# Kernel tuning notes

Hardware: AMD Instinct MI355X
Metric: run time of the kernel (lower is better)

Reference implementation:

```python
import jax, jax.numpy as jnp
import numpy as np

H, RANK, BATCH, T = 1024, 4, 128, 256


def setup_inputs() -> dict:
    key = jax.random.key(0)
    ks = jax.random.split(key, 6)
    s = 1.0 / np.sqrt(H)  # glorot-ish scale for params
    return {
        "x": jax.random.normal(ks[0], (BATCH, T, H), jnp.float32),
        "h0": jnp.zeros((BATCH, H), jnp.float32),
        "d": jax.random.normal(ks[1], (H,), jnp.float32) * s,
        "L": jax.random.normal(ks[2], (H, RANK), jnp.float32) * s,
        "R": jax.random.normal(ks[3], (RANK, H), jnp.float32) * s,
        "B": jax.random.normal(ks[4], (H, H), jnp.float32) * s,
    }


def reference(x, h0, d, L, R, B):
    # Input projection B.T @ x_t for all steps at once (one big GEMM):
    # (B.T @ x)_i = sum_j B[j,i] x[j]  ->  x @ B
    xB = jnp.einsum("bth,hk->btk", x, B)  # [batch, T, H]

    def step(h, u):  # h: [batch, H], u: [batch, H]
        # diagonal + rank-4 low-rank update: d*h + L @ (R @ h) + B.T @ x
        low_rank = (h @ R.T) @ L.T  # [batch, H]
        h = jnp.tanh(d * h + low_rank + u)
        return h, h

    _, hs = jax.lax.scan(step, h0, jnp.swapaxes(xB, 0, 1))  # hs: [T, batch, H]
    return jnp.swapaxes(hs, 0, 1)  # [batch, T, H]
```

## Files before the change

### kernel.cpp

```cpp
#include <hip/hip_runtime.h>
#include <hip/hip_bf16.h>

#define H_DIM  1024
#define RANK_  4
#define BATCH_ 128
#define TSTEPS 256
#define M_DIM  (BATCH_ * TSTEPS)

typedef __bf16 bf16x8 __attribute__((ext_vector_type(8)));
typedef float  floatx4 __attribute__((ext_vector_type(4)));
typedef unsigned short ushortx8 __attribute__((ext_vector_type(8)));

__device__ __forceinline__ unsigned short f2bf(float f) {
    unsigned u = __float_as_uint(f);
    u += 0x7FFFu + ((u >> 16) & 1u);
    return (unsigned short)(u >> 16);
}


__global__ __launch_bounds__(256) void cvt_x_kernel(const float* __restrict__ x,
                                                    unsigned short* __restrict__ xb) {
    size_t i = ((size_t)blockIdx.x * 256 + threadIdx.x) * 8;
    float4 v0 = *(const float4*)(x + i);
    float4 v1 = *(const float4*)(x + i + 4);
    ushortx8 o;
    o[0] = f2bf(v0.x); o[1] = f2bf(v0.y); o[2] = f2bf(v0.z); o[3] = f2bf(v0.w);
    o[4] = f2bf(v1.x); o[5] = f2bf(v1.y); o[6] = f2bf(v1.z); o[7] = f2bf(v1.w);
    *(ushortx8*)(xb + i) = o;
}

__global__ __launch_bounds__(256) void cvt_bt_kernel(const float* __restrict__ B,
                                                     unsigned short* __restrict__ Bt) {
    __shared__ float tl[32][33];
    int tx = threadIdx.x & 31, ty = threadIdx.x >> 5;
    int k0 = blockIdx.y * 32, n0 = blockIdx.x * 32;
#pragma unroll
    for (int j = 0; j < 4; ++j)
        tl[ty + 8 * j][tx] = B[(size_t)(k0 + ty + 8 * j) * H_DIM + n0 + tx];
    __syncthreads();
#pragma unroll
    for (int j = 0; j < 4; ++j)
        Bt[(size_t)(n0 + ty + 8 * j) * H_DIM + k0 + tx] = f2bf(tl[tx][ty + 8 * j]);
}


#define TM 128
#define TN 128
#define BK 64

__global__ __launch_bounds__(256) void gemm_bf16_kernel(const unsigned short* __restrict__ A,
                                                        const unsigned short* __restrict__ Bt,
                                                        float* __restrict__ C) {
    __shared__ unsigned short As[TM * BK];
    __shared__ unsigned short Bs[TN * BK];

    const int tid  = threadIdx.x;
    const int lane = tid & 63;
    const int wid  = tid >> 6;
    const int wm = (wid >> 1) * 64, wn = (wid & 1) * 64;
    const int bm = blockIdx.x >> 3, bn = blockIdx.x & 7;
    const int m0 = bm * TM, n0 = bn * TN;

    const int lr = lane & 15;
    const int lk = (lane >> 4) * 8;

    const unsigned short* ag[4];
    const unsigned short* bg[4];
    unsigned short* asl[4];
    unsigned short* bsl[4];
#pragma unroll
    for (int p = 0; p < 4; ++p) {
        const int ab = wid * 4 + p;
        const int rb = ab >> 1, kb = ab & 1;
        ag[p]  = A  + (size_t)(m0 + rb * 16 + lr) * H_DIM + kb * 32 + lk;
        bg[p]  = Bt + (size_t)(n0 + rb * 16 + lr) * H_DIM + kb * 32 + lk;
        asl[p] = As + ab * 512;
        bsl[p] = Bs + ab * 512;
    }

    floatx4 acc[4][4];
#pragma unroll
    for (int i = 0; i < 4; ++i)
#pragma unroll
        for (int j = 0; j < 4; ++j) acc[i][j] = (floatx4){0.f, 0.f, 0.f, 0.f};

    for (int kt = 0; kt < H_DIM; kt += BK) {
        __syncthreads();
#pragma unroll
        for (int p = 0; p < 4; ++p) {
            __builtin_amdgcn_global_load_lds(
                (const __attribute__((address_space(1))) void*)(ag[p] + kt),
                (__attribute__((address_space(3))) void*)asl[p], 16, 0, 0);
            __builtin_amdgcn_global_load_lds(
                (const __attribute__((address_space(1))) void*)(bg[p] + kt),
                (__attribute__((address_space(3))) void*)bsl[p], 16, 0, 0);
        }
        __syncthreads();
#pragma unroll
        for (int kb = 0; kb < 2; ++kb) {
            bf16x8 af[4], bfv[4];
#pragma unroll
            for (int i = 0; i < 4; ++i) {
                const int rbA = (wm >> 4) + i;
                af[i] = *(const bf16x8*)(As + ((rbA * 2 + kb) << 9) + (lane << 3));
            }
#pragma unroll
            for (int j = 0; j < 4; ++j) {
                const int rbB = (wn >> 4) + j;
                bfv[j] = *(const bf16x8*)(Bs + ((rbB * 2 + kb) << 9) + (lane << 3));
            }
#pragma unroll
            for (int i = 0; i < 4; ++i)
#pragma unroll
                for (int j = 0; j < 4; ++j)
                    acc[i][j] = __builtin_amdgcn_mfma_f32_16x16x32_bf16(af[i], bfv[j], acc[i][j], 0, 0, 0);
        }
    }

    const int cr = (lane >> 4) * 4;
    const int cc = lane & 15;
#pragma unroll
    for (int i = 0; i < 4; ++i)
#pragma unroll
        for (int j = 0; j < 4; ++j) {
            size_t base = (size_t)(m0 + wm + i * 16 + cr) * H_DIM + (n0 + wn + j * 16 + cc);
#pragma unroll
            for (int r = 0; r < 4; ++r)
                C[base + (size_t)r * H_DIM] = acc[i][j][r];
        }
}

__global__ __launch_bounds__(256) void gemm_fp32_fallback(const float* __restrict__ A,
                                                          const float* __restrict__ B,
                                                          float* __restrict__ C) {
    __shared__ float As[64][20];
    __shared__ float Bs[16][68];
    const int tid = threadIdx.x;
    const int bm = blockIdx.x >> 4, bn = blockIdx.x & 15;
    const int m0 = bm * 64, n0 = bn * 64;
    const int tx = (tid & 15) * 4, ty = (tid >> 4) * 4;
    float acc[4][4];
#pragma unroll
    for (int i = 0; i < 4; ++i)
#pragma unroll
        for (int j = 0; j < 4; ++j) acc[i][j] = 0.f;

    for (int kk = 0; kk < H_DIM; kk += 16) {
        float4 av = *(const float4*)(A + (size_t)(m0 + (tid >> 2)) * H_DIM + kk + (tid & 3) * 4);
        float4 bv = *(const float4*)(B + (size_t)(kk + (tid >> 4)) * H_DIM + n0 + (tid & 15) * 4);
        __syncthreads();
        *(float4*)&As[tid >> 2][(tid & 3) * 4] = av;
        *(float4*)&Bs[tid >> 4][(tid & 15) * 4] = bv;
        __syncthreads();
#pragma unroll
        for (int k = 0; k < 16; ++k) {
            float a_[4], b_[4];
#pragma unroll
            for (int i = 0; i < 4; ++i) a_[i] = As[ty + i][k];
#pragma unroll
            for (int j = 0; j < 4; ++j) b_[j] = Bs[k][tx + j];
#pragma unroll
            for (int i = 0; i < 4; ++i)
#pragma unroll
                for (int j = 0; j < 4; ++j) acc[i][j] += a_[i] * b_[j];
        }
    }
#pragma unroll
    for (int i = 0; i < 4; ++i)
#pragma unroll
        for (int j = 0; j < 4; ++j)
            C[(size_t)(m0 + ty + i) * H_DIM + n0 + tx + j] = acc[i][j];
}


__device__ __forceinline__ float tanh_fast(float x) {
    float ax = fabsf(x);
    float e  = __expf(-2.0f * ax);
    float t  = (1.0f - e) * __builtin_amdgcn_rcpf(1.0f + e);
    return copysignf(t, x);
}

__device__ __forceinline__ void barrier_lds_only() {
    asm volatile("s_waitcnt lgkmcnt(0)\n\ts_barrier" ::: "memory");
}

template <int CTRL, int RMASK>
__device__ __forceinline__ float dpp_add(float x) {
    int v = __builtin_amdgcn_update_dpp(0, __float_as_int(x), CTRL, RMASK, 0xf, true);
    return x + __int_as_float(v);
}
__device__ __forceinline__ float wave_sum64(float x) {
    x = dpp_add<0x111, 0xf>(x);
    x = dpp_add<0x112, 0xf>(x);
    x = dpp_add<0x114, 0xf>(x);
    x = dpp_add<0x118, 0xf>(x);
    x = dpp_add<0x142, 0xa>(x);
    x = dpp_add<0x143, 0xc>(x);
    return x;
}

__global__ __launch_bounds__(256) void scan_kernel(const float* __restrict__ h0,
                                                   const float* __restrict__ d,
                                                   const float* __restrict__ Lm,
                                                   const float* __restrict__ Rm,
                                                   float* __restrict__ io) {
    const int b = blockIdx.x, tid = threadIdx.x;
    const int lane = tid & 63, wv = tid >> 6;
    const int e = tid * 4;

    float4 dv4 = *(const float4*)(d + e);
    float dd[4] = {dv4.x, dv4.y, dv4.z, dv4.w};
    float4 hv4 = *(const float4*)(h0 + (size_t)b * H_DIM + e);
    float h[4] = {hv4.x, hv4.y, hv4.z, hv4.w};

    float Lv[4][4], Rv[4][4];
#pragma unroll
    for (int i = 0; i < 4; ++i) {
        float4 t = *(const float4*)(Lm + (size_t)(e + i) * RANK_);
        Lv[i][0] = t.x; Lv[i][1] = t.y; Lv[i][2] = t.z; Lv[i][3] = t.w;
    }
#pragma unroll
    for (int j = 0; j < 4; ++j) {
        float4 t = *(const float4*)(Rm + (size_t)j * H_DIM + e);
        Rv[j][0] = t.x; Rv[j][1] = t.y; Rv[j][2] = t.z; Rv[j][3] = t.w;
    }

    float* iob = io + (size_t)b * TSTEPS * H_DIM + e;
    __shared__ float red[2][4][4];

    float4 u[4];
#pragma unroll
    for (int s = 0; s < 4; ++s) u[s] = *(const float4*)(iob + (size_t)s * H_DIM);

    for (int t = 0; t < TSTEPS; t += 4) {
#pragma unroll
        for (int s = 0; s < 4; ++s) {
            const int tt = t + s;
            float pr[4];
#pragma unroll
            for (int j = 0; j < 4; ++j)
                pr[j] = Rv[j][0] * h[0] + Rv[j][1] * h[1] + Rv[j][2] * h[2] + Rv[j][3] * h[3];
#pragma unroll
            for (int j = 0; j < 4; ++j) pr[j] = wave_sum64(pr[j]);
            if (lane == 63) {
                float4 w; w.x = pr[0]; w.y = pr[1]; w.z = pr[2]; w.w = pr[3];
                *(float4*)&red[s & 1][wv][0] = w;
            }
            barrier_lds_only();
            float4 r0 = *(const float4*)&red[s & 1][0][0];
            float4 r1 = *(const float4*)&red[s & 1][1][0];
            float4 r2 = *(const float4*)&red[s & 1][2][0];
            float4 r3 = *(const float4*)&red[s & 1][3][0];
            float r[4] = {r0.x + r1.x + r2.x + r3.x, r0.y + r1.y + r2.y + r3.y,
                          r0.z + r1.z + r2.z + r3.z, r0.w + r1.w + r2.w + r3.w};

            float uu[4] = {u[s].x, u[s].y, u[s].z, u[s].w};
#pragma unroll
            for (int i = 0; i < 4; ++i) {
                float a = fmaf(dd[i], h[i], uu[i]);
                a += Lv[i][0] * r[0] + Lv[i][1] * r[1] + Lv[i][2] * r[2] + Lv[i][3] * r[3];
                h[i] = tanh_fast(a);
            }
            float4 o; o.x = h[0]; o.y = h[1]; o.z = h[2]; o.w = h[3];
            *(float4*)(iob + (size_t)tt * H_DIM) = o;
            if (tt + 4 < TSTEPS) u[s] = *(const float4*)(iob + (size_t)(tt + 4) * H_DIM);
        }
    }
}


extern "C" void kernel_launch(void* const* d_in, const int* in_sizes, int n_in,
                              void* d_out, int out_size, void* d_ws, size_t ws_size,
                              hipStream_t stream) {
    const float* x  = (const float*)d_in[0];
    const float* h0 = (const float*)d_in[1];
    const float* dd = (const float*)d_in[2];
    const float* L  = (const float*)d_in[3];
    const float* R  = (const float*)d_in[4];
    const float* B  = (const float*)d_in[5];
    float* out = (float*)d_out;

    const size_t need = (size_t)M_DIM * H_DIM * sizeof(unsigned short)
                      + (size_t)H_DIM * H_DIM * sizeof(unsigned short);
    if (ws_size >= need) {
        unsigned short* xb = (unsigned short*)d_ws;
        unsigned short* Bt = xb + (size_t)M_DIM * H_DIM;
        cvt_x_kernel<<<(M_DIM * H_DIM) / (256 * 8), 256, 0, stream>>>(x, xb);
        cvt_bt_kernel<<<dim3(32, 32), 256, 0, stream>>>(B, Bt);
        gemm_bf16_kernel<<<(M_DIM / TM) * (H_DIM / TN), 256, 0, stream>>>(xb, Bt, out);
    } else {
        gemm_fp32_fallback<<<(M_DIM / 64) * (H_DIM / 64), 256, 0, stream>>>(x, B, out);
    }
    scan_kernel<<<BATCH_, 256, 0, stream>>>(h0, dd, L, R, out);
}
```

Measured before the change: 461.9 us.

## Run scan with one wave per batch row and remap GEMM block order

The scan kernel now uses a single 64-lane wave per batch row, with 16 elements per lane. This removes the per-step LDS reduction and s_barrier: the rank-4 projection is reduced with DPP and broadcast via readlane. Output stores are delayed by one step so they overlap the next step's compute. The GEMM block index is also remapped so that consecutive blocks share B tiles across eight M tiles, for better cache reuse. The scan now runs on only 128 waves with higher register pressure, so per-step latency depends on one wave's serial work.

```diff
diff --git a/kernel.cpp b/kernel.cpp
--- a/kernel.cpp
+++ b/kernel.cpp
@@ -58,7 +58,9 @@
     const int lane = tid & 63;
     const int wid  = tid >> 6;
     const int wm = (wid >> 1) * 64, wn = (wid & 1) * 64;
-    const int bm = blockIdx.x >> 3, bn = blockIdx.x & 7;
+    const int g  = blockIdx.x;
+    const int bn = (g >> 3) & 7;
+    const int bm = ((g >> 6) << 3) | (g & 7);
     const int m0 = bm * TM, n0 = bn * TN;
 
     const int lr = lane & 15;
@@ -180,10 +182,6 @@
     return copysignf(t, x);
 }
 
-__device__ __forceinline__ void barrier_lds_only() {
-    asm volatile("s_waitcnt lgkmcnt(0)\n\ts_barrier" ::: "memory");
-}
-
 template <int CTRL, int RMASK>
 __device__ __forceinline__ float dpp_add(float x) {
     int v = __builtin_amdgcn_update_dpp(0, __float_as_int(x), CTRL, RMASK, 0xf, true);
@@ -199,73 +197,109 @@
     return x;
 }
 
-__global__ __launch_bounds__(256) void scan_kernel(const float* __restrict__ h0,
-                                                   const float* __restrict__ d,
-                                                   const float* __restrict__ Lm,
-                                                   const float* __restrict__ Rm,
-                                                   float* __restrict__ io) {
-    const int b = blockIdx.x, tid = threadIdx.x;
-    const int lane = tid & 63, wv = tid >> 6;
-    const int e = tid * 4;
-
-    float4 dv4 = *(const float4*)(d + e);
-    float dd[4] = {dv4.x, dv4.y, dv4.z, dv4.w};
-    float4 hv4 = *(const float4*)(h0 + (size_t)b * H_DIM + e);
-    float h[4] = {hv4.x, hv4.y, hv4.z, hv4.w};
-
-    float Lv[4][4], Rv[4][4];
-#pragma unroll
-    for (int i = 0; i < 4; ++i) {
-        float4 t = *(const float4*)(Lm + (size_t)(e + i) * RANK_);
-        Lv[i][0] = t.x; Lv[i][1] = t.y; Lv[i][2] = t.z; Lv[i][3] = t.w;
-    }
-#pragma unroll
-    for (int j = 0; j < 4; ++j) {
-        float4 t = *(const float4*)(Rm + (size_t)j * H_DIM + e);
-        Rv[j][0] = t.x; Rv[j][1] = t.y; Rv[j][2] = t.z; Rv[j][3] = t.w;
-    }
-
-    float* iob = io + (size_t)b * TSTEPS * H_DIM + e;
-    __shared__ float red[2][4][4];
-
-    float4 u[4];
-#pragma unroll
-    for (int s = 0; s < 4; ++s) u[s] = *(const float4*)(iob + (size_t)s * H_DIM);
+__global__ __launch_bounds__(64, 1) void scan_kernel(const float* __restrict__ h0,
+                                                     const float* __restrict__ d,
+                                                     const float* __restrict__ Lm,
+                                                     const float* __restrict__ Rm,
+                                                     float* __restrict__ io) {
+    const int b    = blockIdx.x;
+    const int lane = threadIdx.x;
+    const int e0   = lane * 4;
+
+    float dd[16], h[16], Lv[16][4], Rv[4][16];
+#pragma unroll
+    for (int c = 0; c < 4; ++c) {
+        float4 t = *(const float4*)(d + c * 256 + e0);
+        dd[c*4+0] = t.x; dd[c*4+1] = t.y; dd[c*4+2] = t.z; dd[c*4+3] = t.w;
+        float4 hh = *(const float4*)(h0 + (size_t)b * H_DIM + c * 256 + e0);
+        h[c*4+0] = hh.x; h[c*4+1] = hh.y; h[c*4+2] = hh.z; h[c*4+3] = hh.w;
+    }
+#pragma unroll
+    for (int c = 0; c < 4; ++c)
+#pragma unroll
+        for (int q = 0; q < 4; ++q) {
+            float4 t = *(const float4*)(Lm + (size_t)(c * 256 + e0 + q) * RANK_);
+            Lv[c*4+q][0] = t.x; Lv[c*4+q][1] = t.y; Lv[c*4+q][2] = t.z; Lv[c*4+q][3] = t.w;
+        }
+#pragma unroll
+    for (int j = 0; j < 4; ++j)
+#pragma unroll
+        for (int c = 0; c < 4; ++c) {
+            float4 t = *(const float4*)(Rm + (size_t)j * H_DIM + c * 256 + e0);
+            Rv[j][c*4+0] = t.x; Rv[j][c*4+1] = t.y; Rv[j][c*4+2] = t.z; Rv[j][c*4+3] = t.w;
+        }
+
+    float* iob = io + (size_t)b * TSTEPS * H_DIM + e0;
+
+    float4 u[4][4];
+#pragma unroll
+    for (int s = 0; s < 4; ++s)
+#pragma unroll
+        for (int c = 0; c < 4; ++c)
+            u[s][c] = *(const float4*)(iob + (size_t)s * H_DIM + c * 256);
+
+    float4 o[4][4];
 
     for (int t = 0; t < TSTEPS; t += 4) {
 #pragma unroll
         for (int s = 0; s < 4; ++s) {
             const int tt = t + s;
+
             float pr[4];
 #pragma unroll
+            for (int j = 0; j < 4; ++j) {
+                float a0 = Rv[j][0] * h[0], a1 = Rv[j][1] * h[1];
+                float a2 = Rv[j][2] * h[2], a3 = Rv[j][3] * h[3];
+#pragma unroll
+                for (int k = 4; k < 16; k += 4) {
+                    a0 = fmaf(Rv[j][k+0], h[k+0], a0);
+                    a1 = fmaf(Rv[j][k+1], h[k+1], a1);
+                    a2 = fmaf(Rv[j][k+2], h[k+2], a2);
+                    a3 = fmaf(Rv[j][k+3], h[k+3], a3);
+                }
+                pr[j] = (a0 + a1) + (a2 + a3);
+            }
+#pragma unroll
+            for (int j = 0; j < 4; ++j) pr[j] = wave_sum64(pr[j]);
+            float r[4];
+#pragma unroll
             for (int j = 0; j < 4; ++j)
-                pr[j] = Rv[j][0] * h[0] + Rv[j][1] * h[1] + Rv[j][2] * h[2] + Rv[j][3] * h[3];
-#pragma unroll
-            for (int j = 0; j < 4; ++j) pr[j] = wave_sum64(pr[j]);
-            if (lane == 63) {
-                float4 w; w.x = pr[0]; w.y = pr[1]; w.z = pr[2]; w.w = pr[3];
-                *(float4*)&red[s & 1][wv][0] = w;
-            }
-            barrier_lds_only();
-            float4 r0 = *(const float4*)&red[s & 1][0][0];
-            float4 r1 = *(const float4*)&red[s & 1][1][0];
-            float4 r2 = *(const float4*)&red[s & 1][2][0];
-            float4 r3 = *(const float4*)&red[s & 1][3][0];
-            float r[4] = {r0.x + r1.x + r2.x + r3.x, r0.y + r1.y + r2.y + r3.y,
-                          r0.z + r1.z + r2.z + r3.z, r0.w + r1.w + r2.w + r3.w};
-
-            float uu[4] = {u[s].x, u[s].y, u[s].z, u[s].w};
-#pragma unroll
-            for (int i = 0; i < 4; ++i) {
-                float a = fmaf(dd[i], h[i], uu[i]);
-                a += Lv[i][0] * r[0] + Lv[i][1] * r[1] + Lv[i][2] * r[2] + Lv[i][3] * r[3];
-                h[i] = tanh_fast(a);
-            }
-            float4 o; o.x = h[0]; o.y = h[1]; o.z = h[2]; o.w = h[3];
-            *(float4*)(iob + (size_t)tt * H_DIM) = o;
-            if (tt + 4 < TSTEPS) u[s] = *(const float4*)(iob + (size_t)(tt + 4) * H_DIM);
-        }
-    }
+                r[j] = __int_as_float(__builtin_amdgcn_readlane(__float_as_int(pr[j]), 63));
+
+            if (tt > 0) {
+                const int tp = tt - 1;
+#pragma unroll
+                for (int c = 0; c < 4; ++c)
+                    *(float4*)(iob + (size_t)tp * H_DIM + c * 256) = o[(tp) & 3][c];
+            }
+
+#pragma unroll
+            for (int c = 0; c < 4; ++c) {
+                float uu[4] = {u[s][c].x, u[s][c].y, u[s][c].z, u[s][c].w};
+#pragma unroll
+                for (int q = 0; q < 4; ++q) {
+                    const int k = c * 4 + q;
+                    float a = fmaf(dd[k], h[k], uu[q]);
+                    a = fmaf(Lv[k][0], r[0], a);
+                    a = fmaf(Lv[k][1], r[1], a);
+                    a = fmaf(Lv[k][2], r[2], a);
+                    a = fmaf(Lv[k][3], r[3], a);
+                    h[k] = tanh_fast(a);
+                }
+                float4 ov; ov.x = h[c*4+0]; ov.y = h[c*4+1]; ov.z = h[c*4+2]; ov.w = h[c*4+3];
+                o[s][c] = ov;
+            }
+
+            if (tt + 4 < TSTEPS) {
+#pragma unroll
+                for (int c = 0; c < 4; ++c)
+                    u[s][c] = *(const float4*)(iob + (size_t)(tt + 4) * H_DIM + c * 256);
+            }
+        }
+    }
+#pragma unroll
+    for (int c = 0; c < 4; ++c)
+        *(float4*)(iob + (size_t)(TSTEPS - 1) * H_DIM + c * 256) = o[3][c];
 }
 
 
@@ -291,5 +325,5 @@
     } else {
         gemm_fp32_fallback<<<(M_DIM / 64) * (H_DIM / 64), 256, 0, stream>>>(x, B, out);
     }
-    scan_kernel<<<BATCH_, 256, 0, stream>>>(h0, dd, L, R, out);
-}
+    scan_kernel<<<BATCH_, 64, 0, stream>>>(h0, dd, L, R, out);
+}
```

Result: slower. 542.8 us (+17.5%).
